# Optimization experiments

Hardware: AMD Instinct MI355X
Metric: run time of the kernel (lower is better)

Reference implementation:

```python
import jax, jax.numpy as jnp
import numpy as np


def setup_inputs() -> dict:
    key = jax.random.key(0)
    k1, k2 = jax.random.split(key)
    a = jax.random.normal(k1, (16384, 64), dtype=jnp.float32)
    b = jax.random.normal(k2, (16384, 64), dtype=jnp.float32)
    return {"a": a, "b": b}


def reference(a, b):
    # torch.cdist(a, b) with p=2: Euclidean distance matrix [N, M]
    # computed via the gram trick: |a|^2 + |b|^2 - 2 a.b
    sq = (
        jnp.sum(a * a, axis=1)[:, None]
        + jnp.sum(b * b, axis=1)[None, :]
        - 2.0 * (a @ b.T)
    )
    dists = jnp.sqrt(jnp.maximum(sq, 0.0))  # [N, M]
    d_ab = jnp.min(dists, axis=0)  # per-b nearest-a distance, [M]
    d_ba = jnp.min(dists, axis=1)  # per-a nearest-b distance, [N]
    return jnp.mean(jnp.concatenate([d_ab, d_ba]))
```

## Files before the change

### kernel.cpp

```cpp
#include <hip/hip_runtime.h>
#include <hip/hip_bf16.h>
#include <cstdint>

#define N_PTS 16384
#define DIM   64
#define BM    128
#define CHUNK 2048
#define NT    (CHUNK / 64)
#define NPANEL (N_PTS / BM)
#define NCHUNK (N_PTS / CHUNK)
#define RED_BLKS 256
#define IPB  (N_PTS / RED_BLKS)

typedef __attribute__((ext_vector_type(8))) short short8;
typedef __attribute__((ext_vector_type(4))) float f32x4;

#define A_BF_OFF  0u
#define B_BF_OFF  ((unsigned)(N_PTS * DIM * 2))
#define A2_OFF    ((unsigned)(2u * N_PTS * DIM * 2))
#define B2_OFF    (A2_OFF + (unsigned)(N_PTS * 4))
#define ROW_OFF   (B2_OFF + (unsigned)(N_PTS * 4))
#define COL_OFF   (ROW_OFF + (unsigned)(NCHUNK * N_PTS * 4))
#define PART_OFF  (COL_OFF + (unsigned)(NPANEL * N_PTS * 4))

__device__ __forceinline__ unsigned f2o(float f) {
    unsigned b = __float_as_uint(f);
    return b ^ (unsigned)((((int)b) >> 31) | 0x80000000);
}
__device__ __forceinline__ float o2f(unsigned u) {
    unsigned b = (u & 0x80000000u) ? (u ^ 0x80000000u) : ~u;
    return __uint_as_float(b);
}
__device__ __forceinline__ unsigned short f2bf(float f) {
    unsigned b = __float_as_uint(f);
    b += 0x7FFFu + ((b >> 16) & 1u);
    return (unsigned short)(b >> 16);
}
__device__ __forceinline__ float min3f(float a, float b, float c) {
    return fminf(fminf(a, b), c);
}

__global__ __launch_bounds__(256) void cd_convert(
    const float* __restrict__ a, const float* __restrict__ b,
    unsigned short* __restrict__ abf, unsigned short* __restrict__ bbf,
    float* __restrict__ a2, float* __restrict__ b2) {
    __shared__ ushort4 T[64][17];
    const int blk = blockIdx.x;
    const bool isB = blk >= (N_PTS / 64);
    const float* src = isB ? b : a;
    unsigned short* dst = isB ? bbf : abf;
    float* nrm = isB ? b2 : a2;
    const int rb = (blk & (N_PTS / 64 - 1)) * 64;
    const int tid = threadIdx.x;
    const float sc = isB ? 1.0f : -2.0f;

    {
        int rg = tid >> 4, part = tid & 15;
        #pragma unroll
        for (int it = 0; it < 4; ++it) {
            int rowl = it * 16 + rg;
            float4 v = ((const float4*)src)[(size_t)(rb + rowl) * 16 + part];
            float s = v.x * v.x + v.y * v.y + v.z * v.z + v.w * v.w;
            s += __shfl_xor(s, 1, 64);
            s += __shfl_xor(s, 2, 64);
            s += __shfl_xor(s, 4, 64);
            s += __shfl_xor(s, 8, 64);
            if (part == 0) nrm[rb + rowl] = s;
            ushort4 u;
            u.x = f2bf(sc * v.x); u.y = f2bf(sc * v.y);
            u.z = f2bf(sc * v.z); u.w = f2bf(sc * v.w);
            T[rowl][part] = u;
        }
    }
    __syncthreads();
    {
        int kgh = tid >> 4, rl0 = tid & 15;
        int kg = kgh >> 1, half = kgh & 1;
        #pragma unroll
        for (int it = 0; it < 4; ++it) {
            int rl = it * 16 + rl0;
            ((ushort4*)dst)[(size_t)(kg * N_PTS + rb + rl) * 2 + half] = T[rl][kgh];
        }
    }
}

__global__ __launch_bounds__(256, 3) void cd_gemm(
    const unsigned short* __restrict__ abf, const unsigned short* __restrict__ bbf,
    const float* __restrict__ a2, const float* __restrict__ b2,
    float* __restrict__ ws_row, float* __restrict__ ws_col) {

    __shared__ unsigned colmin[CHUNK];
    __shared__ unsigned rowmin_s[BM];

    const int tid  = threadIdx.x;
    const int lane = tid & 63;
    const int wid  = tid >> 6;
    const int wm   = wid >> 1;
    const int wn   = wid & 1;
    const int l15  = lane & 15;
    const int l4   = lane >> 4;
    const int cblk = blockIdx.x;
    const int pblk = blockIdx.y;
    const int rowbase = pblk * BM;
    const int colbase = cblk * CHUNK;

    for (int i = tid; i < CHUNK; i += 256) colmin[i] = 0xFFFFFFFFu;
    if (tid < BM) rowmin_s[tid] = 0xFFFFFFFFu;

    short8 af[2][4];
    #pragma unroll
    for (int ks = 0; ks < 2; ++ks)
        #pragma unroll
        for (int m = 0; m < 4; ++m) {
            int arow = rowbase + wm * 64 + m * 16 + l15;
            af[ks][m] = *(const short8*)(abf + (size_t)((ks * 4 + l4) * N_PTS + arow) * 8);
        }
    f32x4 a2v[4];
    #pragma unroll
    for (int m = 0; m < 4; ++m)
        a2v[m] = *(const f32x4*)(a2 + rowbase + wm * 64 + m * 16 + l4 * 4);

    float rowm[16];
    #pragma unroll
    for (int i = 0; i < 16; ++i) rowm[i] = __builtin_inff();

    __syncthreads();

    auto loadB = [&](int t, short8 (&bf)[2][2], float (&bv)[2]) {
        int col0 = colbase + t * 64 + wn * 32;
        #pragma unroll
        for (int n = 0; n < 2; ++n) {
            int col = col0 + n * 16 + l15;
            #pragma unroll
            for (int ks = 0; ks < 2; ++ks)
                bf[ks][n] = *(const short8*)(bbf + (size_t)((ks * 4 + l4) * N_PTS + col) * 8);
            bv[n] = b2[col];
        }
    };

    auto compute = [&](int t, const short8 (&bf)[2][2], const float (&bv)[2]) {
        f32x4 acc[4][2];
        __builtin_amdgcn_s_setprio(1);
        #pragma unroll
        for (int m = 0; m < 4; ++m)
            #pragma unroll
            for (int n = 0; n < 2; ++n)
                acc[m][n] = __builtin_amdgcn_mfma_f32_16x16x32_bf16(af[0][m], bf[0][n], a2v[m], 0, 0, 0);
        #pragma unroll
        for (int m = 0; m < 4; ++m)
            #pragma unroll
            for (int n = 0; n < 2; ++n)
                acc[m][n] = __builtin_amdgcn_mfma_f32_16x16x32_bf16(af[1][m], bf[1][n], acc[m][n], 0, 0, 0);
        __builtin_amdgcn_s_setprio(0);

        float colt[2] = {__builtin_inff(), __builtin_inff()};
        #pragma unroll
        for (int n = 0; n < 2; ++n)
            #pragma unroll
            for (int m = 0; m < 4; ++m) {
                colt[n] = min3f(colt[n], acc[m][n][0], acc[m][n][1]);
                colt[n] = min3f(colt[n], acc[m][n][2], acc[m][n][3]);
            }
        #pragma unroll
        for (int m = 0; m < 4; ++m)
            #pragma unroll
            for (int r = 0; r < 4; ++r)
                rowm[m * 4 + r] = min3f(rowm[m * 4 + r],
                                        acc[m][0][r] + bv[0],
                                        acc[m][1][r] + bv[1]);
        #pragma unroll
        for (int n = 0; n < 2; ++n)
            atomicMin(&colmin[t * 64 + wn * 32 + n * 16 + l15], f2o(colt[n]));
    };

    short8 bfA[2][2], bfB[2][2];
    float bvA[2], bvB[2];
    loadB(0, bfA, bvA);
    for (int t = 0; t < NT; t += 2) {
        loadB(t + 1, bfB, bvB);
        compute(t, bfA, bvA);
        if (t + 2 < NT) loadB(t + 2, bfA, bvA);
        compute(t + 1, bfB, bvB);
    }

    #pragma unroll
    for (int i = 0; i < 16; ++i) {
        float v = rowm[i];
        v = fminf(v, __shfl_xor(v, 1, 64));
        v = fminf(v, __shfl_xor(v, 2, 64));
        v = fminf(v, __shfl_xor(v, 4, 64));
        v = fminf(v, __shfl_xor(v, 8, 64));
        if (l15 == 0)
            atomicMin(&rowmin_s[wm * 64 + (i >> 2) * 16 + l4 * 4 + (i & 3)], f2o(v));
    }
    __syncthreads();

    if (tid < BM)
        ws_row[(size_t)cblk * N_PTS + rowbase + tid] = o2f(rowmin_s[tid]);
    for (int i = tid; i < CHUNK; i += 256)
        ws_col[(size_t)pblk * N_PTS + colbase + i] = o2f(colmin[i]);
}

__global__ __launch_bounds__(256) void cd_reduce(
    const float* __restrict__ ws_row, const float* __restrict__ ws_col,
    const float* __restrict__ b2, float* __restrict__ partial) {
    const int tid = threadIdx.x;
    const int il  = tid & 63;
    const int s   = tid >> 6;
    const int i   = blockIdx.x * IPB + il;

    float cm = __builtin_inff(), rm = __builtin_inff();
    #pragma unroll 8
    for (int p = s * (NPANEL / 4); p < (s + 1) * (NPANEL / 4); ++p)
        cm = fminf(cm, ws_col[(size_t)p * N_PTS + i]);
    #pragma unroll
    for (int c = s * (NCHUNK / 4); c < (s + 1) * (NCHUNK / 4); ++c)
        rm = fminf(rm, ws_row[(size_t)c * N_PTS + i]);

    __shared__ float scm[4][64], srm[4][64];
    scm[s][il] = cm;
    srm[s][il] = rm;
    __syncthreads();

    if (s == 0) {
        cm = fminf(fminf(scm[0][il], scm[1][il]), fminf(scm[2][il], scm[3][il]));
        rm = fminf(fminf(srm[0][il], srm[1][il]), fminf(srm[2][il], srm[3][il]));
        float v = sqrtf(fmaxf(rm, 0.f)) + sqrtf(fmaxf(cm + b2[i], 0.f));
        v += __shfl_xor(v, 1, 64);
        v += __shfl_xor(v, 2, 64);
        v += __shfl_xor(v, 4, 64);
        v += __shfl_xor(v, 8, 64);
        v += __shfl_xor(v, 16, 64);
        v += __shfl_xor(v, 32, 64);
        if (il == 0) partial[blockIdx.x] = v;
    }
}

__global__ __launch_bounds__(256) void cd_final(
    const float* __restrict__ partial, float* __restrict__ out) {
    float s = partial[threadIdx.x];
    s += __shfl_xor(s, 1, 64);
    s += __shfl_xor(s, 2, 64);
    s += __shfl_xor(s, 4, 64);
    s += __shfl_xor(s, 8, 64);
    s += __shfl_xor(s, 16, 64);
    s += __shfl_xor(s, 32, 64);
    __shared__ float w[4];
    if ((threadIdx.x & 63) == 0) w[threadIdx.x >> 6] = s;
    __syncthreads();
    if (threadIdx.x == 0)
        out[0] = (w[0] + w[1] + w[2] + w[3]) * (1.0f / (2.0f * N_PTS));
}

extern "C" void kernel_launch(void* const* d_in, const int* in_sizes, int n_in,
                              void* d_out, int out_size, void* d_ws, size_t ws_size,
                              hipStream_t stream) {
    const float* a = (const float*)d_in[0];
    const float* b = (const float*)d_in[1];
    char* ws = (char*)d_ws;
    unsigned short* abf = (unsigned short*)(ws + A_BF_OFF);
    unsigned short* bbf = (unsigned short*)(ws + B_BF_OFF);
    float* a2     = (float*)(ws + A2_OFF);
    float* b2     = (float*)(ws + B2_OFF);
    float* ws_row = (float*)(ws + ROW_OFF);
    float* ws_col = (float*)(ws + COL_OFF);
    float* part   = (float*)(ws + PART_OFF);

    cd_convert<<<dim3(2 * N_PTS / 64), 256, 0, stream>>>(a, b, abf, bbf, a2, b2);
    cd_gemm<<<dim3(NCHUNK, NPANEL), 256, 0, stream>>>(abf, bbf, a2, b2, ws_row, ws_col);
    cd_reduce<<<dim3(RED_BLKS), 256, 0, stream>>>(ws_row, ws_col, b2, part);
    cd_final<<<1, 256, 0, stream>>>(part, (float*)d_out);
}
```

Before: 60.70 us.

## Reduce column minima via global atomics and fuse final reduction into reduce kernel

The GEMM kernel now atomicMin's its per-chunk column minima directly into one global array instead of writing a full per-panel partial matrix (128 x 16384 floats) that the reduce kernel had to re-read. The convert kernel initializes that array and a counter. The reduce kernel uses a last-block-done counter to compute the final mean, removing the separate final launch. This trades large workspace traffic and a launch for global atomic contention across 128 panels per column.

```diff
diff --git a/kernel.cpp b/kernel.cpp
--- a/kernel.cpp
+++ b/kernel.cpp
@@ -9,8 +9,7 @@
 #define NT    (CHUNK / 64)
 #define NPANEL (N_PTS / BM)
 #define NCHUNK (N_PTS / CHUNK)
-#define RED_BLKS 256
-#define IPB  (N_PTS / RED_BLKS)
+#define RED_BLKS 64
 
 typedef __attribute__((ext_vector_type(8))) short short8;
 typedef __attribute__((ext_vector_type(4))) float f32x4;
@@ -20,8 +19,9 @@
 #define A2_OFF    ((unsigned)(2u * N_PTS * DIM * 2))
 #define B2_OFF    (A2_OFF + (unsigned)(N_PTS * 4))
 #define ROW_OFF   (B2_OFF + (unsigned)(N_PTS * 4))
-#define COL_OFF   (ROW_OFF + (unsigned)(NCHUNK * N_PTS * 4))
-#define PART_OFF  (COL_OFF + (unsigned)(NPANEL * N_PTS * 4))
+#define GCOL_OFF  (ROW_OFF + (unsigned)(NCHUNK * N_PTS * 4))
+#define CNT_OFF   (GCOL_OFF + (unsigned)(N_PTS * 4))
+#define PART_OFF  (CNT_OFF + 256u)
 
 __device__ __forceinline__ unsigned f2o(float f) {
     unsigned b = __float_as_uint(f);
@@ -43,15 +43,20 @@
 __global__ __launch_bounds__(256) void cd_convert(
     const float* __restrict__ a, const float* __restrict__ b,
     unsigned short* __restrict__ abf, unsigned short* __restrict__ bbf,
-    float* __restrict__ a2, float* __restrict__ b2) {
+    float* __restrict__ a2, float* __restrict__ b2,
+    unsigned* __restrict__ gcol, unsigned* __restrict__ counter) {
     __shared__ ushort4 T[64][17];
     const int blk = blockIdx.x;
+    const int tid = threadIdx.x;
+
+    if (blk < (N_PTS / 256)) gcol[blk * 256 + tid] = 0xFFFFFFFFu;
+    if (blk == 64 && tid == 0) *counter = 0u;
+
     const bool isB = blk >= (N_PTS / 64);
     const float* src = isB ? b : a;
     unsigned short* dst = isB ? bbf : abf;
     float* nrm = isB ? b2 : a2;
     const int rb = (blk & (N_PTS / 64 - 1)) * 64;
-    const int tid = threadIdx.x;
     const float sc = isB ? 1.0f : -2.0f;
 
     {
@@ -87,7 +92,7 @@
 __global__ __launch_bounds__(256, 3) void cd_gemm(
     const unsigned short* __restrict__ abf, const unsigned short* __restrict__ bbf,
     const float* __restrict__ a2, const float* __restrict__ b2,
-    float* __restrict__ ws_row, float* __restrict__ ws_col) {
+    float* __restrict__ ws_row, unsigned* __restrict__ gcol) {
 
     __shared__ unsigned colmin[CHUNK];
     __shared__ unsigned rowmin_s[BM];
@@ -198,58 +203,50 @@
     if (tid < BM)
         ws_row[(size_t)cblk * N_PTS + rowbase + tid] = o2f(rowmin_s[tid]);
     for (int i = tid; i < CHUNK; i += 256)
-        ws_col[(size_t)pblk * N_PTS + colbase + i] = o2f(colmin[i]);
+        atomicMin(&gcol[colbase + i], colmin[i]);
 }
 
 __global__ __launch_bounds__(256) void cd_reduce(
-    const float* __restrict__ ws_row, const float* __restrict__ ws_col,
-    const float* __restrict__ b2, float* __restrict__ partial) {
+    const float* __restrict__ ws_row, const unsigned* __restrict__ gcol,
+    const float* __restrict__ b2, float* __restrict__ partial,
+    unsigned* __restrict__ counter, float* __restrict__ out) {
     const int tid = threadIdx.x;
-    const int il  = tid & 63;
-    const int s   = tid >> 6;
-    const int i   = blockIdx.x * IPB + il;
-
-    float cm = __builtin_inff(), rm = __builtin_inff();
-    #pragma unroll 8
-    for (int p = s * (NPANEL / 4); p < (s + 1) * (NPANEL / 4); ++p)
-        cm = fminf(cm, ws_col[(size_t)p * N_PTS + i]);
-    #pragma unroll
-    for (int c = s * (NCHUNK / 4); c < (s + 1) * (NCHUNK / 4); ++c)
-        rm = fminf(rm, ws_row[(size_t)c * N_PTS + i]);
-
-    __shared__ float scm[4][64], srm[4][64];
-    scm[s][il] = cm;
-    srm[s][il] = rm;
-    __syncthreads();
-
-    if (s == 0) {
-        cm = fminf(fminf(scm[0][il], scm[1][il]), fminf(scm[2][il], scm[3][il]));
-        rm = fminf(fminf(srm[0][il], srm[1][il]), fminf(srm[2][il], srm[3][il]));
-        float v = sqrtf(fmaxf(rm, 0.f)) + sqrtf(fmaxf(cm + b2[i], 0.f));
-        v += __shfl_xor(v, 1, 64);
-        v += __shfl_xor(v, 2, 64);
-        v += __shfl_xor(v, 4, 64);
-        v += __shfl_xor(v, 8, 64);
-        v += __shfl_xor(v, 16, 64);
-        v += __shfl_xor(v, 32, 64);
-        if (il == 0) partial[blockIdx.x] = v;
-    }
-}
-
-__global__ __launch_bounds__(256) void cd_final(
-    const float* __restrict__ partial, float* __restrict__ out) {
-    float s = partial[threadIdx.x];
-    s += __shfl_xor(s, 1, 64);
-    s += __shfl_xor(s, 2, 64);
-    s += __shfl_xor(s, 4, 64);
-    s += __shfl_xor(s, 8, 64);
-    s += __shfl_xor(s, 16, 64);
-    s += __shfl_xor(s, 32, 64);
+    const int i = blockIdx.x * 256 + tid;
+
+    float rm = __builtin_inff();
+    #pragma unroll
+    for (int c = 0; c < NCHUNK; ++c) rm = fminf(rm, ws_row[(size_t)c * N_PTS + i]);
+    float cm = o2f(gcol[i]);
+    float v = sqrtf(fmaxf(rm, 0.f)) + sqrtf(fmaxf(cm + b2[i], 0.f));
+    v += __shfl_xor(v, 1, 64);
+    v += __shfl_xor(v, 2, 64);
+    v += __shfl_xor(v, 4, 64);
+    v += __shfl_xor(v, 8, 64);
+    v += __shfl_xor(v, 16, 64);
+    v += __shfl_xor(v, 32, 64);
+
     __shared__ float w[4];
-    if ((threadIdx.x & 63) == 0) w[threadIdx.x >> 6] = s;
-    __syncthreads();
-    if (threadIdx.x == 0)
-        out[0] = (w[0] + w[1] + w[2] + w[3]) * (1.0f / (2.0f * N_PTS));
+    __shared__ bool lastblk;
+    if ((tid & 63) == 0) w[tid >> 6] = v;
+    __syncthreads();
+    if (tid == 0) {
+        partial[blockIdx.x] = w[0] + w[1] + w[2] + w[3];
+        __threadfence();
+        unsigned ret = atomicAdd(counter, 1u);
+        lastblk = (ret == RED_BLKS - 1);
+    }
+    __syncthreads();
+    if (lastblk && tid < 64) {
+        __threadfence();
+        float s = ((volatile float*)partial)[tid];
+        s += __shfl_xor(s, 1, 64);
+        s += __shfl_xor(s, 2, 64);
+        s += __shfl_xor(s, 4, 64);
+        s += __shfl_xor(s, 8, 64);
+        s += __shfl_xor(s, 16, 64);
+        s += __shfl_xor(s, 32, 64);
+        if (tid == 0) out[0] = s * (1.0f / (2.0f * N_PTS));
+    }
 }
 
 extern "C" void kernel_launch(void* const* d_in, const int* in_sizes, int n_in,
@@ -260,14 +257,14 @@
     char* ws = (char*)d_ws;
     unsigned short* abf = (unsigned short*)(ws + A_BF_OFF);
     unsigned short* bbf = (unsigned short*)(ws + B_BF_OFF);
-    float* a2     = (float*)(ws + A2_OFF);
-    float* b2     = (float*)(ws + B2_OFF);
-    float* ws_row = (float*)(ws + ROW_OFF);
-    float* ws_col = (float*)(ws + COL_OFF);
-    float* part   = (float*)(ws + PART_OFF);
-
-    cd_convert<<<dim3(2 * N_PTS / 64), 256, 0, stream>>>(a, b, abf, bbf, a2, b2);
-    cd_gemm<<<dim3(NCHUNK, NPANEL), 256, 0, stream>>>(abf, bbf, a2, b2, ws_row, ws_col);
-    cd_reduce<<<dim3(RED_BLKS), 256, 0, stream>>>(ws_row, ws_col, b2, part);
-    cd_final<<<1, 256, 0, stream>>>(part, (float*)d_out);
-}
+    float* a2      = (float*)(ws + A2_OFF);
+    float* b2      = (float*)(ws + B2_OFF);
+    float* ws_row  = (float*)(ws + ROW_OFF);
+    unsigned* gcol = (unsigned*)(ws + GCOL_OFF);
+    unsigned* cnt  = (unsigned*)(ws + CNT_OFF);
+    float* part    = (float*)(ws + PART_OFF);
+
+    cd_convert<<<dim3(2 * N_PTS / 64), 256, 0, stream>>>(a, b, abf, bbf, a2, b2, gcol, cnt);
+    cd_gemm<<<dim3(NCHUNK, NPANEL), 256, 0, stream>>>(abf, bbf, a2, b2, ws_row, gcol);
+    cd_reduce<<<dim3(RED_BLKS), 256, 0, stream>>>(ws_row, gcol, b2, part, cnt, (float*)d_out);
+}
```

After: 54.98 us. 1.1x faster.
